# Kernel optimization log

Hardware: AMD Instinct MI355X
Metric: run time of the kernel (lower is better)

The kernel has to match this reference:

```python
import jax, jax.numpy as jnp
import numpy as np

B, S, D, VOCAB = 64, 2048, 256, 32000


def setup_inputs() -> dict:
    key = jax.random.key(0)
    k1, k2, k3 = jax.random.split(key, 3)
    chunk = jax.random.randint(k1, (B, S), 0, VOCAB, dtype=jnp.int32)
    encoding = jax.random.normal(k2, (B, S, D), dtype=jnp.float32)
    # idf weights are positive; uniform (0,1] avoids zero-sum pathologies
    idf = jax.random.uniform(k3, (VOCAB,), dtype=jnp.float32, minval=1e-3, maxval=1.0)
    return {"chunk": chunk, "encoding": encoding, "idf": idf}


def reference(chunk, encoding, idf):
    """Batched, fused version of DocumentDualEmbedder.get_doc_embedding.

    chunk:    [B, S] int token ids
    encoding: [B, S, D] transformer outputs
    idf:      [vocab] idf weight table
    returns:  [B, 4*D] (idf-weighted mean | max | min | std)
    """
    seq_len = encoding.shape[1]
    w = idf[chunk]                                  # [B, S] gather
    w = w / jnp.sum(w, axis=1, keepdims=True)       # per-doc normalize
    mean_emb = jnp.einsum('bs,bsd->bd', w, encoding)
    max_emb = jnp.max(encoding, axis=1)
    min_emb = jnp.min(encoding, axis=1)
    # torch.std default: unbiased (divide by S-1)
    mu = jnp.mean(encoding, axis=1, keepdims=True)  # [B, 1, D]
    var = jnp.sum(jnp.square(encoding - mu), axis=1) / (seq_len - 1)
    std_emb = jnp.sqrt(var)
    return jnp.concatenate([mean_emb, max_emb, min_emb, std_emb], axis=-1)
```

## Files before the change

kernel.cpp:

```cpp
#include <hip/hip_runtime.h>

#define BB 64
#define SS 2048
#define DD 256
#define NQ 4
#define DQ (DD / NQ)
#define NT 1024
#define NW (NT / 64)

#define FLT_BIG 3.4028234e38f

typedef float f32x4 __attribute__((ext_vector_type(4)));

__global__ __launch_bounds__(NT) void fused_kernel(
    const int* __restrict__ chunk, const float* __restrict__ enc,
    const float* __restrict__ idf, float* __restrict__ out) {
  const int dq = blockIdx.x;
  const int b = blockIdx.y;
  const int tid = threadIdx.x;
  const int lane = tid & 63;
  const int wid = tid >> 6;
  const int d4 = tid & 15;
  const int srow = tid >> 4;

  __shared__ float sw[SS];
  __shared__ float warr[NW];
  __shared__ float red[NW][16][20];

  const int c0 = chunk[b * SS + tid];
  const int c1 = chunk[b * SS + NT + tid];

  const float* base = enc + ((size_t)b * SS) * DD + dq * DQ + d4 * 4;

  f32x4 bufA[8], bufB[8];

#define LOADG(buf, g)                                                        \
  _Pragma("unroll") for (int k = 0; k < 8; ++k) {                            \
    buf[k] = __builtin_nontemporal_load(                                     \
        (const f32x4*)(base + (size_t)(srow + 64 * (8 * (g) + k)) * DD));    \
  }

  LOADG(bufA, 0)

  float w0 = idf[c0];
  float w1 = idf[c1];
  sw[tid] = w0;
  sw[NT + tid] = w1;
  float wp = w0 + w1;
#pragma unroll
  for (int off = 32; off > 0; off >>= 1) wp += __shfl_down(wp, off, 64);
  if (lane == 0) warr[wid] = wp;
  __syncthreads();

  float swe[4] = {0.f, 0.f, 0.f, 0.f};
  float se[4] = {0.f, 0.f, 0.f, 0.f};
  float se2[4] = {0.f, 0.f, 0.f, 0.f};
  float mx[4], mn[4];
#pragma unroll
  for (int k = 0; k < 4; k++) {
    mx[k] = -FLT_BIG;
    mn[k] = FLT_BIG;
  }

#define PROCG(buf, g)                                                        \
  _Pragma("unroll") for (int k = 0; k < 8; ++k) {                            \
    const int s = srow + 64 * (8 * (g) + k);                                 \
    const float w = sw[s];  \
    _Pragma("unroll") for (int j = 0; j < 4; ++j) {                          \
      const float e = buf[k][j];                                             \
      swe[j] = fmaf(w, e, swe[j]);                                           \
      se[j] += e;                                                            \
      se2[j] = fmaf(e, e, se2[j]);                                           \
      mx[j] = fmaxf(mx[j], e);                                               \
      mn[j] = fminf(mn[j], e);                                               \
    }                                                                        \
  }

  LOADG(bufB, 1)
  PROCG(bufA, 0)
  LOADG(bufA, 2)
  PROCG(bufB, 1)
  LOADG(bufB, 3)
  PROCG(bufA, 2)
  PROCG(bufB, 3)

#undef LOADG
#undef PROCG

#pragma unroll
  for (int j = 0; j < 4; j++) {
    swe[j] += __shfl_xor(swe[j], 32, 64);
    swe[j] += __shfl_xor(swe[j], 16, 64);
    se[j] += __shfl_xor(se[j], 32, 64);
    se[j] += __shfl_xor(se[j], 16, 64);
    se2[j] += __shfl_xor(se2[j], 32, 64);
    se2[j] += __shfl_xor(se2[j], 16, 64);
    mx[j] = fmaxf(mx[j], __shfl_xor(mx[j], 32, 64));
    mx[j] = fmaxf(mx[j], __shfl_xor(mx[j], 16, 64));
    mn[j] = fminf(mn[j], __shfl_xor(mn[j], 32, 64));
    mn[j] = fminf(mn[j], __shfl_xor(mn[j], 16, 64));
  }
  if (lane < 16) {
    float* r = red[wid][lane];
#pragma unroll
    for (int j = 0; j < 4; j++) {
      r[j] = swe[j];
      r[4 + j] = se[j];
      r[8 + j] = se2[j];
      r[12 + j] = mx[j];
      r[16 + j] = mn[j];
    }
  }
  __syncthreads();

  if (tid < DQ) {
    int f4 = tid >> 2, comp = tid & 3;
    float cswe = 0.f, cse = 0.f, cse2 = 0.f, wtot = 0.f;
    float cmx = -FLT_BIG, cmn = FLT_BIG;
#pragma unroll
    for (int wv = 0; wv < NW; wv++) {
      const float* r = red[wv][f4];
      cswe += r[comp];
      cse += r[4 + comp];
      cse2 += r[8 + comp];
      cmx = fmaxf(cmx, r[12 + comp]);
      cmn = fminf(cmn, r[16 + comp]);
      wtot += warr[wv];
    }
    float mu = cse / (float)SS;
    float stdv =
        sqrtf(fmaxf((cse2 - (float)SS * mu * mu) / (float)(SS - 1), 0.f));
    int d = dq * DQ + tid;
    size_t ob = (size_t)b * 4 * DD;
    out[ob + d] = cswe / wtot;
    out[ob + DD + d] = cmx;
    out[ob + 2 * DD + d] = cmn;
    out[ob + 3 * DD + d] = stdv;
  }
}

extern "C" void kernel_launch(void* const* d_in, const int* in_sizes, int n_in,
                              void* d_out, int out_size, void* d_ws,
                              size_t ws_size, hipStream_t stream) {
  const int* chunk = (const int*)d_in[0];
  const float* enc = (const float*)d_in[1];
  const float* idf = (const float*)d_in[2];
  float* out = (float*)d_out;

  fused_kernel<<<dim3(NQ, BB), NT, 0, stream>>>(chunk, enc, idf, out);
}
```

Measured before the change: 185.6 us.

## Split sequence reduction into two-stage kernels with workspace partials

Replaces the single fused kernel, which splits D into four quarters per batch, with a stage1 kernel that splits the sequence into 8 chunks of 256 rows. Each wave reads full 1 KB contiguous rows, and the kernel writes per-chunk partial sums, max, min and weight sums to the workspace. A small stage2 kernel then combines the 8 partials per batch and computes the final outputs. The aim is more, smaller blocks (512 threads, launch bounds allowing 4 per CU) and better row-contiguous memory access, at the cost of an extra launch and a workspace round trip. The old fused path remains as a fallback when the workspace is too small.

```diff
diff --git a/kernel.cpp b/kernel.cpp
--- a/kernel.cpp
+++ b/kernel.cpp
@@ -11,6 +11,151 @@
 #define FLT_BIG 3.4028234e38f
 
 typedef float f32x4 __attribute__((ext_vector_type(4)));
+
+#define S1_ROWS 256
+#define S1_NT 512
+#define S1_NW 8
+#define PART_STRIDE (5 * 256)
+#define WSUM_OFF (BB * 8 * PART_STRIDE)
+
+__global__ __launch_bounds__(S1_NT, 4) void stage1(
+    const int* __restrict__ chunk, const float* __restrict__ enc,
+    const float* __restrict__ idf, float* __restrict__ part) {
+  const int sq = blockIdx.x;
+  const int b = blockIdx.y;
+  const int tid = threadIdx.x;
+  const int lane = tid & 63;
+  const int wid = tid >> 6;
+
+  __shared__ float sw[S1_ROWS];
+  __shared__ float warr[4];
+  __shared__ float red[S1_NW][64][21];
+
+  const int s0 = sq * S1_ROWS;
+  const float* base = enc + ((size_t)b * SS + s0) * DD + lane * 4;
+
+  int c0 = 0;
+  if (tid < S1_ROWS) c0 = chunk[b * SS + s0 + tid];
+
+  f32x4 bufA[8], bufB[8];
+
+#define LOADG(buf, g)                                                       \
+  _Pragma("unroll") for (int k = 0; k < 8; ++k) {                           \
+    buf[k] = __builtin_nontemporal_load(                                    \
+        (const f32x4*)(base + (size_t)(wid + 8 * (8 * (g) + k)) * DD));     \
+  }
+
+  LOADG(bufA, 0)
+
+  if (tid < S1_ROWS) {
+    float w = idf[c0];
+    sw[tid] = w;
+    float wp = w;
+#pragma unroll
+    for (int off = 32; off > 0; off >>= 1) wp += __shfl_down(wp, off, 64);
+    if (lane == 0) warr[wid] = wp;
+  }
+  __syncthreads();
+
+  float swe[4] = {0.f, 0.f, 0.f, 0.f};
+  float se[4] = {0.f, 0.f, 0.f, 0.f};
+  float se2[4] = {0.f, 0.f, 0.f, 0.f};
+  float mx[4], mn[4];
+#pragma unroll
+  for (int k = 0; k < 4; k++) {
+    mx[k] = -FLT_BIG;
+    mn[k] = FLT_BIG;
+  }
+
+#define PROCG(buf, g)                                                       \
+  _Pragma("unroll") for (int k = 0; k < 8; ++k) {                           \
+    const int r = wid + 8 * (8 * (g) + k);                                  \
+    const float w = sw[r];                 \
+    _Pragma("unroll") for (int j = 0; j < 4; ++j) {                         \
+      const float e = buf[k][j];                                            \
+      swe[j] = fmaf(w, e, swe[j]);                                          \
+      se[j] += e;                                                           \
+      se2[j] = fmaf(e, e, se2[j]);                                          \
+      mx[j] = fmaxf(mx[j], e);                                              \
+      mn[j] = fminf(mn[j], e);                                              \
+    }                                                                       \
+  }
+
+  LOADG(bufB, 1)
+  PROCG(bufA, 0)
+  LOADG(bufA, 2)
+  PROCG(bufB, 1)
+  LOADG(bufB, 3)
+  PROCG(bufA, 2)
+  PROCG(bufB, 3)
+
+#undef LOADG
+#undef PROCG
+
+  {
+    float* r = red[wid][lane];
+#pragma unroll
+    for (int j = 0; j < 4; j++) {
+      r[j] = swe[j];
+      r[4 + j] = se[j];
+      r[8 + j] = se2[j];
+      r[12 + j] = mx[j];
+      r[16 + j] = mn[j];
+    }
+  }
+  __syncthreads();
+
+  if (tid < 256) {
+    const int d4 = tid >> 2, comp = tid & 3;
+    float cswe = 0.f, cse = 0.f, cse2 = 0.f;
+    float cmx = -FLT_BIG, cmn = FLT_BIG;
+#pragma unroll
+    for (int wv = 0; wv < S1_NW; wv++) {
+      const float* r = red[wv][d4];
+      cswe += r[comp];
+      cse += r[4 + comp];
+      cse2 += r[8 + comp];
+      cmx = fmaxf(cmx, r[12 + comp]);
+      cmn = fminf(cmn, r[16 + comp]);
+    }
+    float* p = part + (size_t)(b * 8 + sq) * PART_STRIDE;
+    p[tid] = cswe;
+    p[256 + tid] = cse;
+    p[512 + tid] = cse2;
+    p[768 + tid] = cmx;
+    p[1024 + tid] = cmn;
+    if (tid == 0)
+      part[WSUM_OFF + b * 8 + sq] = warr[0] + warr[1] + warr[2] + warr[3];
+  }
+}
+
+__global__ __launch_bounds__(256) void stage2(const float* __restrict__ part,
+                                              float* __restrict__ out) {
+  const int b = blockIdx.x;
+  const int d = threadIdx.x;
+  const float* pb = part + (size_t)b * 8 * PART_STRIDE;
+  const float* ws = part + WSUM_OFF + b * 8;
+  float swe = 0.f, se = 0.f, se2 = 0.f, wtot = 0.f;
+  float mx = -FLT_BIG, mn = FLT_BIG;
+#pragma unroll
+  for (int sq = 0; sq < 8; sq++) {
+    const float* p = pb + sq * PART_STRIDE;
+    swe += p[d];
+    se += p[256 + d];
+    se2 += p[512 + d];
+    mx = fmaxf(mx, p[768 + d]);
+    mn = fminf(mn, p[1024 + d]);
+    wtot += ws[sq];
+  }
+  float mu = se / (float)SS;
+  float stdv =
+      sqrtf(fmaxf((se2 - (float)SS * mu * mu) / (float)(SS - 1), 0.f));
+  size_t ob = (size_t)b * 4 * DD;
+  out[ob + d] = swe / wtot;
+  out[ob + DD + d] = mx;
+  out[ob + 2 * DD + d] = mn;
+  out[ob + 3 * DD + d] = stdv;
+}
 
 __global__ __launch_bounds__(NT) void fused_kernel(
     const int* __restrict__ chunk, const float* __restrict__ enc,
@@ -34,10 +179,10 @@
 
   f32x4 bufA[8], bufB[8];
 
-#define LOADG(buf, g)                                                        \
-  _Pragma("unroll") for (int k = 0; k < 8; ++k) {                            \
-    buf[k] = __builtin_nontemporal_load(                                     \
-        (const f32x4*)(base + (size_t)(srow + 64 * (8 * (g) + k)) * DD));    \
+#define LOADG(buf, g)                                                       \
+  _Pragma("unroll") for (int k = 0; k < 8; ++k) {                           \
+    buf[k] = __builtin_nontemporal_load(                                    \
+        (const f32x4*)(base + (size_t)(srow + 64 * (8 * (g) + k)) * DD));   \
   }
 
   LOADG(bufA, 0)
@@ -62,18 +207,18 @@
     mn[k] = FLT_BIG;
   }
 
-#define PROCG(buf, g)                                                        \
-  _Pragma("unroll") for (int k = 0; k < 8; ++k) {                            \
-    const int s = srow + 64 * (8 * (g) + k);                                 \
-    const float w = sw[s];  \
-    _Pragma("unroll") for (int j = 0; j < 4; ++j) {                          \
-      const float e = buf[k][j];                                             \
-      swe[j] = fmaf(w, e, swe[j]);                                           \
-      se[j] += e;                                                            \
-      se2[j] = fmaf(e, e, se2[j]);                                           \
-      mx[j] = fmaxf(mx[j], e);                                               \
-      mn[j] = fminf(mn[j], e);                                               \
-    }                                                                        \
+#define PROCG(buf, g)                                                       \
+  _Pragma("unroll") for (int k = 0; k < 8; ++k) {                           \
+    const int s = srow + 64 * (8 * (g) + k);                                \
+    const float w = sw[s];                                                  \
+    _Pragma("unroll") for (int j = 0; j < 4; ++j) {                         \
+      const float e = buf[k][j];                                            \
+      swe[j] = fmaf(w, e, swe[j]);                                          \
+      se[j] += e;                                                           \
+      se2[j] = fmaf(e, e, se2[j]);                                          \
+      mx[j] = fmaxf(mx[j], e);                                              \
+      mn[j] = fminf(mn[j], e);                                              \
+    }                                                                       \
   }
 
   LOADG(bufB, 1)
@@ -147,5 +292,12 @@
   const float* idf = (const float*)d_in[2];
   float* out = (float*)d_out;
 
-  fused_kernel<<<dim3(NQ, BB), NT, 0, stream>>>(chunk, enc, idf, out);
+  const size_t need = (size_t)(WSUM_OFF + BB * 8) * sizeof(float);
+  if (ws_size >= need && d_ws != nullptr) {
+    float* part = (float*)d_ws;
+    stage1<<<dim3(8, BB), S1_NT, 0, stream>>>(chunk, enc, idf, part);
+    stage2<<<dim3(BB), 256, 0, stream>>>(part, out);
+  } else {
+    fused_kernel<<<dim3(NQ, BB), NT, 0, stream>>>(chunk, enc, idf, out);
+  }
 }
```

Result: slower. 190.1 us (+2.4%).
